# Optimization experiments

Hardware: AMD Instinct MI355X
Metric: run time of the kernel (lower is better)

Reference implementation:

```python
import jax, jax.numpy as jnp
import numpy as np

EMBED = 1024
HEADS = 16
HEAD_DIM = EMBED // HEADS
B, S = 4, 1024


def setup_inputs() -> dict:
    key = jax.random.key(0)
    ks = jax.random.split(key, 8)
    return {
        "values": jax.random.normal(ks[0], (B, S, EMBED), dtype=jnp.float32),
        "keys": jax.random.normal(ks[1], (B, S, EMBED), dtype=jnp.float32),
        "query": jax.random.normal(ks[2], (B, S, EMBED), dtype=jnp.float32),
        "mask": jax.random.randint(ks[3], (B, 1, S, S), 0, 2, dtype=jnp.int32),
        "Wv": jax.random.normal(ks[4], (HEAD_DIM, HEAD_DIM), dtype=jnp.float32) / np.sqrt(HEAD_DIM),
        "Wq": jax.random.normal(ks[5], (HEAD_DIM, HEAD_DIM), dtype=jnp.float32) / np.sqrt(HEAD_DIM),
        "Wk": jax.random.normal(ks[6], (HEAD_DIM, HEAD_DIM), dtype=jnp.float32) / np.sqrt(HEAD_DIM),
        "Wu": jax.random.normal(ks[7], (EMBED, EMBED), dtype=jnp.float32) / np.sqrt(EMBED),
        "bu": jnp.zeros((EMBED,), dtype=jnp.float32),
    }


def reference(values, keys, query, mask, Wv, Wq, Wk, Wu, bu):
    n, s, _ = query.shape
    # split heads: [B, S, H, D]
    v = values.reshape(n, s, HEADS, HEAD_DIM)
    k = keys.reshape(n, s, HEADS, HEAD_DIM)
    q = query.reshape(n, s, HEADS, HEAD_DIM)
    # per-head linear (shared weight across heads); torch Linear: x @ W.T
    v = jnp.einsum("nshd,ed->nshe", v, Wv)
    k = jnp.einsum("nshd,ed->nshe", k, Wk)
    q = jnp.einsum("nshd,ed->nshe", q, Wq)
    # scores: [B, H, Q, K]
    dot = jnp.einsum("nqhd,nkhd->nhqk", q, k)
    dot = jnp.where(mask == 0, jnp.float32(-1e20), dot)
    # NOTE: original scales by sqrt(embed_size), not sqrt(head_dim)
    attn = jax.nn.softmax(dot / jnp.sqrt(jnp.float32(EMBED)), axis=3)
    out = jnp.einsum("nhql,nlhd->nqhd", attn, v)
    out = out.reshape(n, s, EMBED)
    return out @ Wu.T + bu
```

## Files before the change

### kernel.cpp

```cpp
#include <hip/hip_runtime.h>
#include <hip/hip_bf16.h>

#define EMBED 1024
#define HEADS 16
#define HDIM  64
#define BATCH 4
#define SEQ   1024

typedef __attribute__((ext_vector_type(8))) short  short8;
typedef __attribute__((ext_vector_type(4))) short  short4v;
typedef __attribute__((ext_vector_type(4))) float  float4v;
typedef __attribute__((ext_vector_type(8))) float  float8;
typedef __attribute__((ext_vector_type(2))) __bf16 bf16x2;
typedef __attribute__((ext_vector_type(8))) __bf16 bf16x8;

static __device__ __forceinline__ float4v mfma16(short4v a, short4v b, float4v c) {
#if defined(__HIP_DEVICE_COMPILE__) && __has_builtin(__builtin_amdgcn_mfma_f32_16x16x16bf16_1k)
  return __builtin_amdgcn_mfma_f32_16x16x16bf16_1k(a, b, c, 0, 0, 0);
#else
  float4v d;
  asm("v_mfma_f32_16x16x16_bf16 %0, %1, %2, %3"
      : "=v"(d)
      : "v"(a), "v"(b), "v"(c));
  return d;
#endif
}

static __device__ __forceinline__ short cvt1(float f) {
  return __builtin_bit_cast(short, (__bf16)f);
}

static __device__ __forceinline__ unsigned pkbf(float a, float b) {
  bf16x2 v; v[0] = (__bf16)a; v[1] = (__bf16)b;
  return __builtin_bit_cast(unsigned, v);
}

static __device__ __forceinline__ short8 cvt8(const float* p) {
  float4v a = *(const float4v*)p;
  float4v b = *(const float4v*)(p + 4);
  float8 f = __builtin_shufflevector(a, b, 0, 1, 2, 3, 4, 5, 6, 7);
  bf16x8 bb = __builtin_convertvector(f, bf16x8);
  return __builtin_bit_cast(short8, bb);
}

#define QSCL 0.04508422002778011f

__global__ __launch_bounds__(256) void k_pre(
    const float* __restrict__ values, const float* __restrict__ keys,
    const float* __restrict__ query,
    const float* __restrict__ Wv, const float* __restrict__ Wq,
    const float* __restrict__ Wk, const float* __restrict__ Wu,
    const int* __restrict__ mask,
    short* __restrict__ qp, short* __restrict__ kp, short* __restrict__ vpT,
    unsigned* __restrict__ mbits, short* __restrict__ wub) {
  const int b = blockIdx.x;
  const int t = threadIdx.x;
  if (b < 1536) {
    const int l = t & 63, lr = l & 15, g = l >> 4;
    const int wbase = (b * 4 + (t >> 6)) * 2;
#pragma unroll
    for (int it = 0; it < 2; ++it) {
      const int u = wbase + it;
      const int z = u >> 12;
      const int rem = u & 4095;
      const int h = rem & 15;
      const int r0 = (rem >> 4) * 16;
      const float* in_; const float* Wm;
      if (z == 0)      { in_ = query;  Wm = Wq; }
      else if (z == 1) { in_ = keys;   Wm = Wk; }
      else             { in_ = values; Wm = Wv; }
      const int n = r0 >> 10, s0 = r0 & 1023;
      const int nh = n * HEADS + h;

      float4v acc[4];
#pragma unroll
      for (int nt = 0; nt < 4; ++nt) acc[nt] = (float4v){0.f, 0.f, 0.f, 0.f};
#pragma unroll
      for (int kb = 0; kb < 2; ++kb) {
        short8 af = cvt8(in_ + (size_t)(r0 + lr) * EMBED + h * HDIM + kb * 32 + g * 8);
#pragma unroll
        for (int nt = 0; nt < 4; ++nt) {
          short8 bf = cvt8(Wm + (size_t)(nt * 16 + lr) * HDIM + kb * 32 + g * 8);
          acc[nt] = __builtin_amdgcn_mfma_f32_16x16x32_bf16(af, bf, acc[nt], 0, 0, 0);
        }
      }
      if (z == 2) {
        const int s = s0 + g * 4;
        const int kk = s & 63;
        const int pos = ((kk >> 5) & 1) * 32 + ((kk >> 2) & 3) * 8 + ((kk >> 4) & 1) * 4;
#pragma unroll
        for (int nt = 0; nt < 4; ++nt) {
          short4v r;
          r[0]=cvt1(acc[nt][0]); r[1]=cvt1(acc[nt][1]);
          r[2]=cvt1(acc[nt][2]); r[3]=cvt1(acc[nt][3]);
          *(short4v*)(vpT + (size_t)(nh * HDIM + nt * 16 + lr) * SEQ + (s & ~63) + pos) = r;
        }
      } else {
        short* outp = (z == 0) ? qp : kp;
        const float scl = (z == 0) ? QSCL : 1.0f;
#pragma unroll
        for (int nt = 0; nt < 4; ++nt)
#pragma unroll
          for (int i = 0; i < 4; ++i)
            outp[(size_t)(nh * SEQ + s0 + g * 4 + i) * HDIM + nt * 16 + lr] =
                cvt1(acc[nt][i] * scl);
      }
    }
  } else if (b < 2560) {
    const int tid0 = (b - 1536) * 256 + t;
    const int l = t & 63;
#pragma unroll
    for (int it = 0; it < 16; ++it) {
      int tid = tid0 + it * 262144;
      int v = mask[tid];
      unsigned long long bal = __ballot(v != 0);
      if ((l & 31) == 0) mbits[tid >> 5] = (unsigned)(bal >> (l & 32));
    }
  } else {
    const int base = (b - 2560) * 256 + t;
#pragma unroll
    for (int it = 0; it < 16; ++it) {
      int i4 = (base + it * 16384) * 4;
      float4v v = *(const float4v*)(Wu + i4);
      short4v r; r[0]=cvt1(v[0]); r[1]=cvt1(v[1]); r[2]=cvt1(v[2]); r[3]=cvt1(v[3]);
      *(short4v*)(wub + i4) = r;
    }
  }
}

__global__ __launch_bounds__(256, 4) void k_attn(
    const short* __restrict__ qp, const short* __restrict__ kp,
    const short* __restrict__ vpT, const unsigned* __restrict__ mbits,
    short* __restrict__ ao) {
  const int bid = blockIdx.x;
  const int work = (bid & 7) * 128 + (bid >> 3);
  const int qt = work & 15, grp = work >> 4;
  const int h = grp & 15, n = grp >> 4;

  const int t256 = threadIdx.x;
  const int w = t256 >> 6, l = t256 & 63, lr = l & 15, g = l >> 4;
  const int nh = n * HEADS + h;
  const int q0 = qt * 64 + w * 16;
  const short* qb  = qp  + (size_t)nh * SEQ * HDIM;
  const short* kbp = kp  + (size_t)nh * SEQ * HDIM;
  const short* vb  = vpT + (size_t)nh * HDIM * SEQ;
  const unsigned* mrow = mbits + (size_t)(n * SEQ + q0 + lr) * 32;

  __shared__ __align__(16) short kls0[4096], kls1[4096];
  __shared__ __align__(16) short vls0[4096], vls1[4096];

  const int s0 = t256, s1 = t256 + 256;
  const int r0s = s0 >> 3, c0s = s0 & 7, r1s = s1 >> 3, c1s = s1 & 7;
  const int ld0 = r0s * 64 + ((c0s ^ (r0s & 7)) << 3);
  const int ld1 = r1s * 64 + ((c1s ^ (r1s & 7)) << 3);

  const int e = lr & 7;
  const int base0 = lr * 64 + ((g ^ e) << 3);
  const int base1 = lr * 64 + (((4 + g) ^ e) << 3);

  const short8 qf0 = *(const short8*)(qb + (q0 + lr) * HDIM + g * 8);
  const short8 qf1 = *(const short8*)(qb + (q0 + lr) * HDIM + 32 + g * 8);

  float4v accd[4];
#pragma unroll
  for (int dt = 0; dt < 4; ++dt) accd[dt] = (float4v){0.f, 0.f, 0.f, 0.f};
  float l_i = 0.f;

  auto issue = [&](int tile, short8& K0, short8& K1, short8& V0, short8& V1) {
    const int kn = tile * 64;
    K0 = *(const short8*)(kbp + kn * 64 + s0 * 8);
    K1 = *(const short8*)(kbp + kn * 64 + s1 * 8);
    V0 = *(const short8*)(vb + (size_t)r0s * SEQ + kn + c0s * 8);
    V1 = *(const short8*)(vb + (size_t)r1s * SEQ + kn + c1s * 8);
  };
  auto publish = [&](short* Kd, short* Vd, short8 K0, short8 K1, short8 V0, short8 V1) {
    *(short8*)(Kd + ld0) = K0;
    *(short8*)(Kd + ld1) = K1;
    *(short8*)(Vd + ld0) = V0;
    *(short8*)(Vd + ld1) = V1;
  };
  auto tilec = [&](const short* Kb, const short* Vb, int t) {
    float4v sT[4];
#pragma unroll
    for (int a = 0; a < 4; ++a) {
      short8 kf0 = *(const short8*)(Kb + a * 1024 + base0);
      short8 kf1 = *(const short8*)(Kb + a * 1024 + base1);
      float4v z = (float4v){0.f, 0.f, 0.f, 0.f};
      z = __builtin_amdgcn_mfma_f32_16x16x32_bf16(kf0, qf0, z, 0, 0, 0);
      sT[a] = __builtin_amdgcn_mfma_f32_16x16x32_bf16(kf1, qf1, z, 0, 0, 0);
    }
    uint2 mw = *(const uint2*)(mrow + 2 * t);
    const unsigned t0m = mw.x >> (g * 4);
    const unsigned t1m = mw.y >> (g * 4);
    short4v pb[4];
    float psum = 0.f;
#pragma unroll
    for (int a = 0; a < 4; ++a) {
      unsigned ta = ((a & 2) ? t1m : t0m) >> ((a & 1) * 16);
      float p0 = exp2f(sT[a][0]); p0 = (ta & 1u) ? p0 : 0.f;
      float p1 = exp2f(sT[a][1]); p1 = (ta & 2u) ? p1 : 0.f;
      float p2 = exp2f(sT[a][2]); p2 = (ta & 4u) ? p2 : 0.f;
      float p3 = exp2f(sT[a][3]); p3 = (ta & 8u) ? p3 : 0.f;
      psum += (p0 + p1) + (p2 + p3);
      uint2 u; u.x = pkbf(p0, p1); u.y = pkbf(p2, p3);
      __builtin_memcpy(&pb[a], &u, 8);
    }
    l_i += psum;
#pragma unroll
    for (int dt = 0; dt < 4; ++dt) {
#pragma unroll
      for (int h2 = 0; h2 < 2; ++h2) {
        short8 vf = *(const short8*)(Vb + dt * 1024 + (h2 ? base1 : base0));
        short4v lo = __builtin_shufflevector(vf, vf, 0, 1, 2, 3);
        short4v hi = __builtin_shufflevector(vf, vf, 4, 5, 6, 7);
        accd[dt] = mfma16(lo, pb[2 * h2], accd[dt]);
        accd[dt] = mfma16(hi, pb[2 * h2 + 1], accd[dt]);
      }
    }
  };

  short8 aK0, aK1, aV0, aV1;
  short8 bK0, bK1, bV0, bV1;

  issue(0, aK0, aK1, aV0, aV1);
  publish(kls0, vls0, aK0, aK1, aV0, aV1);
  issue(1, bK0, bK1, bV0, bV1);
  __syncthreads();

  for (int tp = 0; tp < 8; ++tp) {
    if (tp < 7) issue(2 * tp + 2, aK0, aK1, aV0, aV1);
    tilec(kls0, vls0, 2 * tp);
    publish(kls1, vls1, bK0, bK1, bV0, bV1);
    __syncthreads();
    if (tp < 7) issue(2 * tp + 3, bK0, bK1, bV0, bV1);
    tilec(kls1, vls1, 2 * tp + 1);
    if (tp < 7) {
      publish(kls0, vls0, aK0, aK1, aV0, aV1);
      __syncthreads();
    }
  }

  l_i += __shfl_xor(l_i, 16, 64);
  l_i += __shfl_xor(l_i, 32, 64);
  float inv = 1.f / fmaxf(l_i, 1e-35f);
  short* aorow = ao + (size_t)(n * SEQ + q0 + lr) * EMBED + h * HDIM;
#pragma unroll
  for (int dt = 0; dt < 4; ++dt) {
    short4v r;
    r[0] = cvt1(accd[dt][0] * inv);
    r[1] = cvt1(accd[dt][1] * inv);
    r[2] = cvt1(accd[dt][2] * inv);
    r[3] = cvt1(accd[dt][3] * inv);
    *(short4v*)(aorow + dt * 16 + g * 4) = r;
  }
}

__global__ __launch_bounds__(512, 1) void k_gemm(
    const short* __restrict__ ao, const short* __restrict__ wub,
    const float* __restrict__ bu, float* __restrict__ out) {
  const int r0 = blockIdx.x * 128, c0 = blockIdx.y * 128;
  const int t = threadIdx.x;
  const int w = t >> 6, l = t & 63, lr = l & 15, g = l >> 4;
  const int wr = w >> 2, wc = w & 3;

  __shared__ __align__(16) short als[2][128 * 64];
  __shared__ __align__(16) short bls[2][128 * 64];

  const int ar0 = t >> 3, ac0 = t & 7;
  const int ar1 = (t + 512) >> 3, ac1 = (t + 512) & 7;
  const int ld0 = ar0 * 64 + ((ac0 ^ (ar0 & 7)) << 3);
  const int ld1 = ar1 * 64 + ((ac1 ^ (ar1 & 7)) << 3);
  const short* agp0 = ao  + (size_t)(r0 + ar0) * EMBED + ac0 * 8;
  const short* agp1 = ao  + (size_t)(r0 + ar1) * EMBED + ac1 * 8;
  const short* bgp0 = wub + (size_t)(c0 + ar0) * EMBED + ac0 * 8;
  const short* bgp1 = wub + (size_t)(c0 + ar1) * EMBED + ac1 * 8;

  int aoff[4][2], boff[2][2];
#pragma unroll
  for (int fr = 0; fr < 4; ++fr) {
    const int ra = wr * 64 + fr * 16 + lr;
#pragma unroll
    for (int kk = 0; kk < 2; ++kk)
      aoff[fr][kk] = ra * 64 + (((kk * 4 + g) ^ (ra & 7)) << 3);
  }
#pragma unroll
  for (int fc = 0; fc < 2; ++fc) {
    const int rb = wc * 32 + fc * 16 + lr;
#pragma unroll
    for (int kk = 0; kk < 2; ++kk)
      boff[fc][kk] = rb * 64 + (((kk * 4 + g) ^ (rb & 7)) << 3);
  }

  float4v acc[4][2];
#pragma unroll
  for (int fr = 0; fr < 4; ++fr)
#pragma unroll
    for (int fc = 0; fc < 2; ++fc) acc[fr][fc] = (float4v){0.f, 0.f, 0.f, 0.f};

  {
    short8 a0 = *(const short8*)agp0;
    short8 a1 = *(const short8*)agp1;
    short8 b0 = *(const short8*)bgp0;
    short8 b1 = *(const short8*)bgp1;
    *(short8*)(&als[0][0] + ld0) = a0;
    *(short8*)(&als[0][0] + ld1) = a1;
    *(short8*)(&bls[0][0] + ld0) = b0;
    *(short8*)(&bls[0][0] + ld1) = b1;
  }
  __syncthreads();

#pragma unroll 2
  for (int tt = 0; tt < 16; ++tt) {
    const int cur = tt & 1, nxt = cur ^ 1;
    short8 sA0, sA1, sB0, sB1;
    if (tt < 15) {
      const int kb = (tt + 1) * 64;
      sA0 = *(const short8*)(agp0 + kb);
      sA1 = *(const short8*)(agp1 + kb);
      sB0 = *(const short8*)(bgp0 + kb);
      sB1 = *(const short8*)(bgp1 + kb);
    }
#pragma unroll
    for (int kk = 0; kk < 2; ++kk) {
      short8 bf0 = *(const short8*)(&bls[cur][0] + boff[0][kk]);
      short8 bf1 = *(const short8*)(&bls[cur][0] + boff[1][kk]);
#pragma unroll
      for (int fr = 0; fr < 4; ++fr) {
        short8 af = *(const short8*)(&als[cur][0] + aoff[fr][kk]);
        acc[fr][0] = __builtin_amdgcn_mfma_f32_16x16x32_bf16(af, bf0, acc[fr][0], 0, 0, 0);
        acc[fr][1] = __builtin_amdgcn_mfma_f32_16x16x32_bf16(af, bf1, acc[fr][1], 0, 0, 0);
      }
    }
    if (tt < 15) {
      *(short8*)(&als[nxt][0] + ld0) = sA0;
      *(short8*)(&als[nxt][0] + ld1) = sA1;
      *(short8*)(&bls[nxt][0] + ld0) = sB0;
      *(short8*)(&bls[nxt][0] + ld1) = sB1;
      __syncthreads();
    }
  }

#pragma unroll
  for (int fc = 0; fc < 2; ++fc) {
    const int col = c0 + wc * 32 + fc * 16 + lr;
    const float bv = bu[col];
#pragma unroll
    for (int fr = 0; fr < 4; ++fr)
#pragma unroll
      for (int i = 0; i < 4; ++i) {
        const int row = r0 + wr * 64 + fr * 16 + g * 4 + i;
        out[(size_t)row * EMBED + col] = acc[fr][fc][i] + bv;
      }
  }
}

extern "C" void kernel_launch(void* const* d_in, const int* in_sizes, int n_in,
                              void* d_out, int out_size, void* d_ws, size_t ws_size,
                              hipStream_t stream) {
  const float* values = (const float*)d_in[0];
  const float* keys   = (const float*)d_in[1];
  const float* query  = (const float*)d_in[2];
  const int*   mask   = (const int*)d_in[3];
  const float* Wv     = (const float*)d_in[4];
  const float* Wq     = (const float*)d_in[5];
  const float* Wk     = (const float*)d_in[6];
  const float* Wu     = (const float*)d_in[7];
  const float* bu     = (const float*)d_in[8];
  float* out = (float*)d_out;

  char* ws = (char*)d_ws;
  short* qp  = (short*)ws;
  short* kp  = qp + (1u << 22);
  short* vpT = kp + (1u << 22);
  short* ao  = vpT + (1u << 22);
  unsigned* mbits = (unsigned*)(ws + (32u << 20));
  short* wub = (short*)(ws + (32u << 20) + (512u << 10));

  k_pre<<<dim3(2624), 256, 0, stream>>>(values, keys, query, Wv, Wq, Wk, Wu,
                                        mask, qp, kp, vpT, mbits, wub);
  k_attn<<<dim3(1024), 256, 0, stream>>>(qp, kp, vpT, mbits, ao);
  k_gemm<<<dim3(32, 8), 512, 0, stream>>>(ao, wub, bu, out);
}
```

Before: 88.80 us.

## Use 16x16x32 MFMA for PV and compute row sums via MFMA with ones

The P·V product now uses the wider 16x16x32 bf16 MFMA instead of pairs of 16x16x16 MFMAs. To make this work, the key rows are permuted when written out and the mask bit extraction is changed to match. The softmax denominator is accumulated by an MFMA against a vector of ones instead of scalar adds and cross-lane shuffles. This cuts the MFMA instruction count and the VALU reduction work, at the cost of a more intricate permuted K layout and an extra MFMA pair per tile.

```diff
diff --git a/kernel.cpp b/kernel.cpp
--- a/kernel.cpp
+++ b/kernel.cpp
@@ -13,18 +13,6 @@
 typedef __attribute__((ext_vector_type(8))) float  float8;
 typedef __attribute__((ext_vector_type(2))) __bf16 bf16x2;
 typedef __attribute__((ext_vector_type(8))) __bf16 bf16x8;
-
-static __device__ __forceinline__ float4v mfma16(short4v a, short4v b, float4v c) {
-#if defined(__HIP_DEVICE_COMPILE__) && __has_builtin(__builtin_amdgcn_mfma_f32_16x16x16bf16_1k)
-  return __builtin_amdgcn_mfma_f32_16x16x16bf16_1k(a, b, c, 0, 0, 0);
-#else
-  float4v d;
-  asm("v_mfma_f32_16x16x16_bf16 %0, %1, %2, %3"
-      : "=v"(d)
-      : "v"(a), "v"(b), "v"(c));
-  return d;
-#endif
-}
 
 static __device__ __forceinline__ short cvt1(float f) {
   return __builtin_bit_cast(short, (__bf16)f);
@@ -85,25 +73,28 @@
         }
       }
       if (z == 2) {
-        const int s = s0 + g * 4;
-        const int kk = s & 63;
-        const int pos = ((kk >> 5) & 1) * 32 + ((kk >> 2) & 3) * 8 + ((kk >> 4) & 1) * 4;
 #pragma unroll
         for (int nt = 0; nt < 4; ++nt) {
           short4v r;
           r[0]=cvt1(acc[nt][0]); r[1]=cvt1(acc[nt][1]);
           r[2]=cvt1(acc[nt][2]); r[3]=cvt1(acc[nt][3]);
-          *(short4v*)(vpT + (size_t)(nh * HDIM + nt * 16 + lr) * SEQ + (s & ~63) + pos) = r;
+          *(short4v*)(vpT + (size_t)(nh * HDIM + nt * 16 + lr) * SEQ + s0 + g * 4) = r;
         }
       } else {
         short* outp = (z == 0) ? qp : kp;
         const float scl = (z == 0) ? QSCL : 1.0f;
+        const int b8 = ((s0 >> 4) & 1) * 8;
+        const int rbase = s0 & ~31;
 #pragma unroll
         for (int nt = 0; nt < 4; ++nt)
 #pragma unroll
-          for (int i = 0; i < 4; ++i)
-            outp[(size_t)(nh * SEQ + s0 + g * 4 + i) * HDIM + nt * 16 + lr] =
+          for (int i = 0; i < 4; ++i) {
+            const int row = (z == 0)
+                ? (s0 + g * 4 + i)
+                : (rbase + (g & 1) * 16 + b8 + (g >> 1) * 4 + i);
+            outp[(size_t)(nh * SEQ + row) * HDIM + nt * 16 + lr] =
                 cvt1(acc[nt][i] * scl);
+          }
       }
     }
   } else if (b < 2560) {
@@ -161,10 +152,13 @@
   const short8 qf0 = *(const short8*)(qb + (q0 + lr) * HDIM + g * 8);
   const short8 qf1 = *(const short8*)(qb + (q0 + lr) * HDIM + 32 + g * 8);
 
+  const short8 ones8 = {0x3F80, 0x3F80, 0x3F80, 0x3F80,
+                        0x3F80, 0x3F80, 0x3F80, 0x3F80};
+
   float4v accd[4];
 #pragma unroll
   for (int dt = 0; dt < 4; ++dt) accd[dt] = (float4v){0.f, 0.f, 0.f, 0.f};
-  float l_i = 0.f;
+  float4v lacc = (float4v){0.f, 0.f, 0.f, 0.f};
 
   auto issue = [&](int tile, short8& K0, short8& K1, short8& V0, short8& V1) {
     const int kn = tile * 64;
@@ -190,32 +184,30 @@
       sT[a] = __builtin_amdgcn_mfma_f32_16x16x32_bf16(kf1, qf1, z, 0, 0, 0);
     }
     uint2 mw = *(const uint2*)(mrow + 2 * t);
-    const unsigned t0m = mw.x >> (g * 4);
-    const unsigned t1m = mw.y >> (g * 4);
-    short4v pb[4];
-    float psum = 0.f;
+    const unsigned t0 = mw.x >> (g * 8);
+    const unsigned t1 = mw.y >> (g * 8);
+    unsigned dwf[8];
 #pragma unroll
     for (int a = 0; a < 4; ++a) {
-      unsigned ta = ((a & 2) ? t1m : t0m) >> ((a & 1) * 16);
+      unsigned ta = ((a & 2) ? t1 : t0) >> ((a & 1) * 4);
       float p0 = exp2f(sT[a][0]); p0 = (ta & 1u) ? p0 : 0.f;
       float p1 = exp2f(sT[a][1]); p1 = (ta & 2u) ? p1 : 0.f;
       float p2 = exp2f(sT[a][2]); p2 = (ta & 4u) ? p2 : 0.f;
       float p3 = exp2f(sT[a][3]); p3 = (ta & 8u) ? p3 : 0.f;
-      psum += (p0 + p1) + (p2 + p3);
-      uint2 u; u.x = pkbf(p0, p1); u.y = pkbf(p2, p3);
-      __builtin_memcpy(&pb[a], &u, 8);
-    }
-    l_i += psum;
+      dwf[a * 2]     = pkbf(p0, p1);
+      dwf[a * 2 + 1] = pkbf(p2, p3);
+    }
+    short8 pbw0, pbw1;
+    __builtin_memcpy(&pbw0, &dwf[0], 16);
+    __builtin_memcpy(&pbw1, &dwf[4], 16);
+    lacc = __builtin_amdgcn_mfma_f32_16x16x32_bf16(ones8, pbw0, lacc, 0, 0, 0);
+    lacc = __builtin_amdgcn_mfma_f32_16x16x32_bf16(ones8, pbw1, lacc, 0, 0, 0);
 #pragma unroll
     for (int dt = 0; dt < 4; ++dt) {
-#pragma unroll
-      for (int h2 = 0; h2 < 2; ++h2) {
-        short8 vf = *(const short8*)(Vb + dt * 1024 + (h2 ? base1 : base0));
-        short4v lo = __builtin_shufflevector(vf, vf, 0, 1, 2, 3);
-        short4v hi = __builtin_shufflevector(vf, vf, 4, 5, 6, 7);
-        accd[dt] = mfma16(lo, pb[2 * h2], accd[dt]);
-        accd[dt] = mfma16(hi, pb[2 * h2 + 1], accd[dt]);
-      }
+      short8 vf0 = *(const short8*)(Vb + dt * 1024 + base0);
+      accd[dt] = __builtin_amdgcn_mfma_f32_16x16x32_bf16(vf0, pbw0, accd[dt], 0, 0, 0);
+      short8 vf1 = *(const short8*)(Vb + dt * 1024 + base1);
+      accd[dt] = __builtin_amdgcn_mfma_f32_16x16x32_bf16(vf1, pbw1, accd[dt], 0, 0, 0);
     }
   };
 
@@ -240,9 +232,7 @@
     }
   }
 
-  l_i += __shfl_xor(l_i, 16, 64);
-  l_i += __shfl_xor(l_i, 32, 64);
-  float inv = 1.f / fmaxf(l_i, 1e-35f);
+  float inv = 1.f / fmaxf(lacc[0], 1e-35f);
   short* aorow = ao + (size_t)(n * SEQ + q0 + lr) * EMBED + h * HDIM;
 #pragma unroll
   for (int dt = 0; dt < 4; ++dt) {
```

After: 85.28 us. 1.04x faster.
